# Kernel optimization log

Hardware: AMD Instinct MI355X
Metric: run time of the kernel (lower is better)

Reference implementation:

```python
import jax, jax.numpy as jnp
import numpy as np

# Assumptions from DCalhas/eeg_to_fmri repo layers:
#  - RandomFourierFeatures: z = cos(x @ W + b) followed by layer normalization
#    over the feature axis (normalization='layer'), W/b trainable.
#  - Sinusoids: elementwise sin(x).

B, D, T, L = 64, 512, 1024, 512

def _layer_norm(x, eps=1e-5):
    mu = jnp.mean(x, axis=-1, keepdims=True)
    var = jnp.var(x, axis=-1, keepdims=True)
    return (x - mu) * jax.lax.rsqrt(var + eps)

def setup_inputs() -> dict:
    key = jax.random.key(0)
    ks = jax.random.split(key, 12)
    s = 1.0 / np.sqrt(L)
    return {
        "x": jax.random.normal(ks[0], (B, D, T), jnp.float32),
        "rff_w": jax.random.normal(ks[1], (D, L), jnp.float32) * (1.0 / np.sqrt(D)),
        "rff_b": jax.random.uniform(ks[2], (L,), jnp.float32, 0.0, 2.0 * np.pi),
        "weight_input": jax.random.normal(ks[3], (L, L), jnp.float32) * s,
        "weight_forget": jax.random.normal(ks[4], (L, L), jnp.float32) * s,
        "weight_context": jax.random.normal(ks[5], (L, L), jnp.float32) * s,
        "recurrent_input": jax.random.normal(ks[6], (L, L), jnp.float32) * s,
        "recurrent_forget": jax.random.normal(ks[7], (L, L), jnp.float32) * s,
        "recurrent_context": jax.random.normal(ks[8], (L, L), jnp.float32) * s,
        "bias_input": jnp.zeros((L,), jnp.float32),
        "bias_forget": jnp.zeros((L,), jnp.float32),
        "bias_context": jnp.zeros((L,), jnp.float32),
        "init_latent": jax.random.normal(ks[9], (1, 1, L), jnp.float32) * s,
        "init_context": jax.random.normal(ks[10], (1, 1, L), jnp.float32) * s,
    }

def reference(x, rff_w, rff_b, weight_input, weight_forget, weight_context,
              recurrent_input, recurrent_forget, recurrent_context,
              bias_input, bias_forget, bias_context, init_latent, init_context):
    b = x.shape[0]
    xt = jnp.transpose(x, (0, 2, 1))                      # [B,T,D]
    z = _layer_norm(jnp.cos(xt @ rff_w + rff_b))          # [B,T,L]
    # hidden_states[t+1] = z_t in the original loop, so the "recurrent" input
    # at step t is z_{t-1} (init_latent at t=0). Gates are thus batchable.
    z_prev = jnp.concatenate(
        [jnp.broadcast_to(init_latent, (b, 1, z.shape[2])), z[:, :-1]], axis=1)
    i = jax.nn.sigmoid(z @ weight_input + z_prev @ recurrent_input + bias_input)
    f = jax.nn.sigmoid(z @ weight_forget + z_prev @ recurrent_forget + bias_forget)
    g = jnp.tanh(z @ weight_context + z_prev @ recurrent_context + bias_context)
    o = jnp.sin(z)                                        # Sinusoids gate

    c0 = jnp.broadcast_to(init_context[:, 0], (b, z.shape[2]))  # [B,L]
    def step(c_prev, gates):
        i_t, f_t, g_t, o_t = gates
        c_t = f_t * c_prev + i_t * g_t
        return c_t, o_t * c_t
    xs = tuple(jnp.transpose(a, (1, 0, 2)) for a in (i, f, g, o))  # time-major
    _, h = jax.lax.scan(step, c0, xs)                     # [T,B,L]
    return jnp.transpose(h, (1, 2, 0))                    # [B,L,T]
```

## Files before the change

kernel.cpp:

```cpp
#include <hip/hip_runtime.h>
#include <hip/hip_bf16.h>
#include <hip/hip_fp16.h>
#include <cstdint>
#include <cstddef>


typedef float f32x4 __attribute__((ext_vector_type(4)));
typedef short s16x8 __attribute__((ext_vector_type(8)));

__device__ __forceinline__ void gload_lds16(const void* g, void* l) {
  __builtin_amdgcn_global_load_lds(
      (const __attribute__((address_space(1))) void*)g,
      (__attribute__((address_space(3))) void*)l, 16, 0, 0);
}
__device__ __forceinline__ ushort f2bf(float f) {
  uint32_t u = __float_as_uint(f);
  return (ushort)((u + 0x7FFF + ((u >> 16) & 1)) >> 16);
}
__device__ __forceinline__ float bf2f(ushort s) {
  return __uint_as_float(((uint32_t)s) << 16);
}
__device__ __forceinline__ ushort f2h(float f) {
  return __half_as_ushort(__float2half(f));
}
__device__ __forceinline__ float h2f(ushort s) {
  return __half2float(__ushort_as_half(s));
}

#define MF(d, a, b) d = __builtin_amdgcn_mfma_f32_16x16x32_bf16(a, b, d, 0, 0, 0);

__global__ __launch_bounds__(256) void transpose_cvt(
    const float* __restrict__ src, ushort* __restrict__ dst, int ld)
{
  __shared__ float tile[32][33];
  const int c0 = blockIdx.x * 32, r0 = blockIdx.y * 32;
  const int tx = threadIdx.x & 31, ty = threadIdx.x >> 5;
#pragma unroll
  for (int i = 0; i < 4; ++i)
    tile[ty + i * 8][tx] = src[(size_t)(r0 + ty + i * 8) * 512 + c0 + tx];
  __syncthreads();
#pragma unroll
  for (int i = 0; i < 4; ++i)
    dst[(size_t)(c0 + ty + i * 8) * ld + r0 + tx] = f2bf(tile[tx][ty + i * 8]);
}

__global__ __launch_bounds__(256) void transpose6(
    const float* __restrict__ s0, const float* __restrict__ s1,
    const float* __restrict__ s2, const float* __restrict__ s3,
    const float* __restrict__ s4, const float* __restrict__ s5,
    const float* __restrict__ il, ushort* __restrict__ W2t,
    ushort* __restrict__ ilb)
{
  const int z = blockIdx.z;
  if (z == 6) {
    if (blockIdx.x == 0 && blockIdx.y == 0) {
      ilb[threadIdx.x] = f2bf(il[threadIdx.x]);
      ilb[threadIdx.x + 256] = f2bf(il[threadIdx.x + 256]);
    }
    return;
  }
  const float* src = z == 0 ? s0 : z == 1 ? s1 : z == 2 ? s2
                   : z == 3 ? s3 : z == 4 ? s4 : s5;
  ushort* dst = W2t + (size_t)(z >> 1) * 512 * 1024 + (z & 1) * 512;
  __shared__ float tile[32][33];
  const int c0 = blockIdx.x * 32, r0 = blockIdx.y * 32;
  const int tx = threadIdx.x & 31, ty = threadIdx.x >> 5;
#pragma unroll
  for (int i = 0; i < 4; ++i)
    tile[ty + i * 8][tx] = src[(size_t)(r0 + ty + i * 8) * 512 + c0 + tx];
  __syncthreads();
#pragma unroll
  for (int i = 0; i < 4; ++i)
    dst[(size_t)(c0 + ty + i * 8) * 1024 + r0 + tx] = f2bf(tile[tx][ty + i * 8]);
}

__global__ __launch_bounds__(256) void transpose_x(
    const float* __restrict__ x, ushort* __restrict__ xt)
{
  __shared__ float tile[64][68];
  const int b = blockIdx.z;
  const int t0 = blockIdx.x * 64, d0 = blockIdx.y * 64;
  const float* src = x + ((size_t)b * 512 + d0) * 1024 + t0;
  const int lr_ = threadIdx.x >> 4, lc4 = (threadIdx.x & 15) * 4;
#pragma unroll
  for (int p = 0; p < 4; ++p) {
    const float4 v = *(const float4*)(src + (size_t)(lr_ + p * 16) * 1024 + lc4);
    *(float4*)&tile[lr_ + p * 16][lc4] = v;
  }
  __syncthreads();
  const int tt = threadIdx.x >> 2, dc = (threadIdx.x & 3) * 16;
  ushort* dst = xt + ((size_t)b * 1024 + t0 + tt) * 512 + d0 + dc;
  uint4 o1, o2;
  o1.x = (uint)f2bf(tile[dc + 0][tt]) | ((uint)f2bf(tile[dc + 1][tt]) << 16);
  o1.y = (uint)f2bf(tile[dc + 2][tt]) | ((uint)f2bf(tile[dc + 3][tt]) << 16);
  o1.z = (uint)f2bf(tile[dc + 4][tt]) | ((uint)f2bf(tile[dc + 5][tt]) << 16);
  o1.w = (uint)f2bf(tile[dc + 6][tt]) | ((uint)f2bf(tile[dc + 7][tt]) << 16);
  o2.x = (uint)f2bf(tile[dc + 8][tt]) | ((uint)f2bf(tile[dc + 9][tt]) << 16);
  o2.y = (uint)f2bf(tile[dc + 10][tt]) | ((uint)f2bf(tile[dc + 11][tt]) << 16);
  o2.z = (uint)f2bf(tile[dc + 12][tt]) | ((uint)f2bf(tile[dc + 13][tt]) << 16);
  o2.w = (uint)f2bf(tile[dc + 14][tt]) | ((uint)f2bf(tile[dc + 15][tt]) << 16);
  *(uint4*)(dst) = o1;
  *(uint4*)(dst + 8) = o2;
}

__global__ __launch_bounds__(256, 2) void k1_mfma(
    const ushort* __restrict__ A, const ushort* __restrict__ Bt,
    const float* __restrict__ bias, ushort* __restrict__ U)
{
  __shared__ __align__(16) short As[128 * 64];
  __shared__ __align__(16) short Bs[128 * 64];
  const int tid = threadIdx.x;
  const int lane = tid & 63, wid = tid >> 6;
  const int orig = blockIdx.x;
  const int swz = (orig & 7) * 256 + (orig >> 3);
  const int n0 = (swz & 3) * 128, r0 = (swz >> 2) * 128;
  const int wr = wid >> 1, wc = wid & 1;
  const int fr = lane & 15, fq = lane >> 4;
  const int lr = lane >> 3;
  const int swz_el = ((lane & 7) ^ lr) * 8;

  const int RA = r0 + wid * 32 + lr;
  const ushort* pa0 = A + (size_t)(RA)      * 512 + swz_el;
  const ushort* pa1 = A + (size_t)(RA + 8)  * 512 + swz_el;
  const ushort* pa2 = A + (size_t)(RA + 16) * 512 + swz_el;
  const ushort* pa3 = A + (size_t)(RA + 24) * 512 + swz_el;
  const int RB = n0 + wid * 32 + lr;
  const ushort* pb0 = Bt + (size_t)(RB)      * 512 + swz_el;
  const ushort* pb1 = Bt + (size_t)(RB + 8)  * 512 + swz_el;
  const ushort* pb2 = Bt + (size_t)(RB + 16) * 512 + swz_el;
  const ushort* pb3 = Bt + (size_t)(RB + 24) * 512 + swz_el;
  char* dA = (char*)As + wid * 4096;
  char* dB = (char*)Bs + wid * 4096;

  const int so0 = fr * 64 + ((fq)     ^ (fr & 7)) * 8;
  const int so1 = fr * 64 + ((4 + fq) ^ (fr & 7)) * 8;

  f32x4 c00 = {0.f,0.f,0.f,0.f}, c01 = c00, c02 = c00, c03 = c00,
        c10 = c00, c11 = c00, c12 = c00, c13 = c00,
        c20 = c00, c21 = c00, c22 = c00, c23 = c00,
        c30 = c00, c31 = c00, c32 = c00, c33 = c00;

  for (int k0 = 0; k0 < 512; k0 += 64) {
    gload_lds16(pa0 + k0, dA);        gload_lds16(pa1 + k0, dA + 1024);
    gload_lds16(pa2 + k0, dA + 2048); gload_lds16(pa3 + k0, dA + 3072);
    gload_lds16(pb0 + k0, dB);        gload_lds16(pb1 + k0, dB + 1024);
    gload_lds16(pb2 + k0, dB + 2048); gload_lds16(pb3 + k0, dB + 3072);
    __syncthreads();
    const s16x8 a00 = *(const s16x8*)&As[wr * 4096 + 0 * 1024 + so0];
    const s16x8 a01 = *(const s16x8*)&As[wr * 4096 + 0 * 1024 + so1];
    const s16x8 a10 = *(const s16x8*)&As[wr * 4096 + 1 * 1024 + so0];
    const s16x8 a11 = *(const s16x8*)&As[wr * 4096 + 1 * 1024 + so1];
    const s16x8 a20 = *(const s16x8*)&As[wr * 4096 + 2 * 1024 + so0];
    const s16x8 a21 = *(const s16x8*)&As[wr * 4096 + 2 * 1024 + so1];
    const s16x8 a30 = *(const s16x8*)&As[wr * 4096 + 3 * 1024 + so0];
    const s16x8 a31 = *(const s16x8*)&As[wr * 4096 + 3 * 1024 + so1];
    const s16x8 b00 = *(const s16x8*)&Bs[wc * 4096 + 0 * 1024 + so0];
    const s16x8 b01 = *(const s16x8*)&Bs[wc * 4096 + 0 * 1024 + so1];
    const s16x8 b10 = *(const s16x8*)&Bs[wc * 4096 + 1 * 1024 + so0];
    const s16x8 b11 = *(const s16x8*)&Bs[wc * 4096 + 1 * 1024 + so1];
    const s16x8 b20 = *(const s16x8*)&Bs[wc * 4096 + 2 * 1024 + so0];
    const s16x8 b21 = *(const s16x8*)&Bs[wc * 4096 + 2 * 1024 + so1];
    const s16x8 b30 = *(const s16x8*)&Bs[wc * 4096 + 3 * 1024 + so0];
    const s16x8 b31 = *(const s16x8*)&Bs[wc * 4096 + 3 * 1024 + so1];
    MF(c00, a00, b00) MF(c01, a00, b10) MF(c02, a00, b20) MF(c03, a00, b30)
    MF(c10, a10, b00) MF(c11, a10, b10) MF(c12, a10, b20) MF(c13, a10, b30)
    MF(c20, a20, b00) MF(c21, a20, b10) MF(c22, a20, b20) MF(c23, a20, b30)
    MF(c30, a30, b00) MF(c31, a30, b10) MF(c32, a30, b20) MF(c33, a30, b30)
    MF(c00, a01, b01) MF(c01, a01, b11) MF(c02, a01, b21) MF(c03, a01, b31)
    MF(c10, a11, b01) MF(c11, a11, b11) MF(c12, a11, b21) MF(c13, a11, b31)
    MF(c20, a21, b01) MF(c21, a21, b11) MF(c22, a21, b21) MF(c23, a21, b31)
    MF(c30, a31, b01) MF(c31, a31, b11) MF(c32, a31, b21) MF(c33, a31, b31)
    __syncthreads();
  }

#define EPI1(cmn, m_, n_) { \
    const int col = n0 + wc * 64 + n_ * 16 + fr; \
    const float bv = bias[col]; \
    const int rbase = r0 + wr * 64 + m_ * 16 + fq * 4; \
    _Pragma("unroll") for (int j = 0; j < 4; ++j) \
      U[(size_t)(rbase + j) * 512 + col] = f2bf(cosf(cmn[j] + bv)); }
  EPI1(c00, 0, 0) EPI1(c01, 0, 1) EPI1(c02, 0, 2) EPI1(c03, 0, 3)
  EPI1(c10, 1, 0) EPI1(c11, 1, 1) EPI1(c12, 1, 2) EPI1(c13, 1, 3)
  EPI1(c20, 2, 0) EPI1(c21, 2, 1) EPI1(c22, 2, 2) EPI1(c23, 2, 3)
  EPI1(c30, 3, 0) EPI1(c31, 3, 1) EPI1(c32, 3, 2) EPI1(c33, 3, 3)
#undef EPI1
}

__global__ __launch_bounds__(256) void ln_rows(
    const ushort* __restrict__ U, ushort* __restrict__ Z)
{
  const int row = blockIdx.x * 4 + (threadIdx.x >> 6);
  const int lane = threadIdx.x & 63;
  const size_t base = (size_t)row * 512 + lane * 8;
  const uint4 pk = *(const uint4*)(U + base);
  float v[8];
  v[0] = bf2f(pk.x & 0xffff); v[1] = bf2f(pk.x >> 16);
  v[2] = bf2f(pk.y & 0xffff); v[3] = bf2f(pk.y >> 16);
  v[4] = bf2f(pk.z & 0xffff); v[5] = bf2f(pk.z >> 16);
  v[6] = bf2f(pk.w & 0xffff); v[7] = bf2f(pk.w >> 16);
  float s = 0.f, s2 = 0.f;
#pragma unroll
  for (int j = 0; j < 8; ++j) { s += v[j]; s2 += v[j] * v[j]; }
#pragma unroll
  for (int m = 1; m < 64; m <<= 1) { s += __shfl_xor(s, m); s2 += __shfl_xor(s2, m); }
  const float mean = s * (1.f / 512.f);
  const float var = s2 * (1.f / 512.f) - mean * mean;
  const float inv = rsqrtf(var + 1e-5f);
  uint4 o;
  o.x = (uint)f2bf((v[0] - mean) * inv) | ((uint)f2bf((v[1] - mean) * inv) << 16);
  o.y = (uint)f2bf((v[2] - mean) * inv) | ((uint)f2bf((v[3] - mean) * inv) << 16);
  o.z = (uint)f2bf((v[4] - mean) * inv) | ((uint)f2bf((v[5] - mean) * inv) << 16);
  o.w = (uint)f2bf((v[6] - mean) * inv) | ((uint)f2bf((v[7] - mean) * inv) << 16);
  *(uint4*)(Z + base) = o;
}

__global__ __launch_bounds__(256, 2) void k2_mfma(
    const ushort* __restrict__ Z, const ushort* __restrict__ Wt,
    const ushort* __restrict__ IL,
    const float* __restrict__ b0v, const float* __restrict__ b1v,
    const float* __restrict__ b2v,
    ushort* __restrict__ gates, int tc, int Tc, int nwg)
{
  __shared__ __align__(16) short As[128 * 64];
  __shared__ __align__(16) short Bs[128 * 64];
  const int tid = threadIdx.x;
  const int lane = tid & 63, wid = tid >> 6;
  const int cpx = nwg >> 3;
  const int orig = blockIdx.x;
  const int swz = (orig & 7) * cpx + (orig >> 3);
  const int bx = swz % 12, by = swz / 12;
  const int nb = Tc >> 7;
  const int b = by / nb, tb = by % nb;
  const int r0g = b * 1024 + tc + tb * 128;
  const int r0c = b * Tc + tb * 128;
  const int n0 = bx * 128;
  const int wr = wid >> 1, wc = wid & 1;
  const int fr = lane & 15, fq = lane >> 4;
  const int lr = lane >> 3;
  const int swz_el = ((lane & 7) ^ lr) * 8;

  const int R0 = r0g + wid * 32 + lr;
  const ushort* pa0 = Z + (size_t)(R0)      * 512 + swz_el;
  const ushort* pa1 = Z + (size_t)(R0 + 8)  * 512 + swz_el;
  const ushort* pa2 = Z + (size_t)(R0 + 16) * 512 + swz_el;
  const ushort* pa3 = Z + (size_t)(R0 + 24) * 512 + swz_el;
  const ushort* ph0 = ((((R0)      & 1023) == 0) ? IL : (Z + (size_t)(R0 - 1)  * 512)) + swz_el;
  const ushort* ph1 = ((((R0 + 8)  & 1023) == 0) ? IL : (Z + (size_t)(R0 + 7)  * 512)) + swz_el;
  const ushort* ph2 = ((((R0 + 16) & 1023) == 0) ? IL : (Z + (size_t)(R0 + 15) * 512)) + swz_el;
  const ushort* ph3 = ((((R0 + 24) & 1023) == 0) ? IL : (Z + (size_t)(R0 + 23) * 512)) + swz_el;
  const int RB = n0 + wid * 32 + lr;
  const ushort* pb0 = Wt + (size_t)(RB)      * 1024 + swz_el;
  const ushort* pb1 = Wt + (size_t)(RB + 8)  * 1024 + swz_el;
  const ushort* pb2 = Wt + (size_t)(RB + 16) * 1024 + swz_el;
  const ushort* pb3 = Wt + (size_t)(RB + 24) * 1024 + swz_el;
  char* dA = (char*)As + wid * 4096;
  char* dB = (char*)Bs + wid * 4096;

  const int so0 = fr * 64 + ((fq)     ^ (fr & 7)) * 8;
  const int so1 = fr * 64 + ((4 + fq) ^ (fr & 7)) * 8;

  f32x4 c00 = {0.f,0.f,0.f,0.f}, c01 = c00, c02 = c00, c03 = c00,
        c10 = c00, c11 = c00, c12 = c00, c13 = c00,
        c20 = c00, c21 = c00, c22 = c00, c23 = c00,
        c30 = c00, c31 = c00, c32 = c00, c33 = c00;

#define K2BODY \
    __syncthreads(); \
    { \
    const s16x8 a00 = *(const s16x8*)&As[wr * 4096 + 0 * 1024 + so0]; \
    const s16x8 a01 = *(const s16x8*)&As[wr * 4096 + 0 * 1024 + so1]; \
    const s16x8 a10 = *(const s16x8*)&As[wr * 4096 + 1 * 1024 + so0]; \
    const s16x8 a11 = *(const s16x8*)&As[wr * 4096 + 1 * 1024 + so1]; \
    const s16x8 a20 = *(const s16x8*)&As[wr * 4096 + 2 * 1024 + so0]; \
    const s16x8 a21 = *(const s16x8*)&As[wr * 4096 + 2 * 1024 + so1]; \
    const s16x8 a30 = *(const s16x8*)&As[wr * 4096 + 3 * 1024 + so0]; \
    const s16x8 a31 = *(const s16x8*)&As[wr * 4096 + 3 * 1024 + so1]; \
    const s16x8 b00 = *(const s16x8*)&Bs[wc * 4096 + 0 * 1024 + so0]; \
    const s16x8 b01 = *(const s16x8*)&Bs[wc * 4096 + 0 * 1024 + so1]; \
    const s16x8 b10 = *(const s16x8*)&Bs[wc * 4096 + 1 * 1024 + so0]; \
    const s16x8 b11 = *(const s16x8*)&Bs[wc * 4096 + 1 * 1024 + so1]; \
    const s16x8 b20 = *(const s16x8*)&Bs[wc * 4096 + 2 * 1024 + so0]; \
    const s16x8 b21 = *(const s16x8*)&Bs[wc * 4096 + 2 * 1024 + so1]; \
    const s16x8 b30 = *(const s16x8*)&Bs[wc * 4096 + 3 * 1024 + so0]; \
    const s16x8 b31 = *(const s16x8*)&Bs[wc * 4096 + 3 * 1024 + so1]; \
    MF(c00, a00, b00) MF(c01, a00, b10) MF(c02, a00, b20) MF(c03, a00, b30) \
    MF(c10, a10, b00) MF(c11, a10, b10) MF(c12, a10, b20) MF(c13, a10, b30) \
    MF(c20, a20, b00) MF(c21, a20, b10) MF(c22, a20, b20) MF(c23, a20, b30) \
    MF(c30, a30, b00) MF(c31, a30, b10) MF(c32, a30, b20) MF(c33, a30, b30) \
    MF(c00, a01, b01) MF(c01, a01, b11) MF(c02, a01, b21) MF(c03, a01, b31) \
    MF(c10, a11, b01) MF(c11, a11, b11) MF(c12, a11, b21) MF(c13, a11, b31) \
    MF(c20, a21, b01) MF(c21, a21, b11) MF(c22, a21, b21) MF(c23, a21, b31) \
    MF(c30, a31, b01) MF(c31, a31, b11) MF(c32, a31, b21) MF(c33, a31, b31) \
    } \
    __syncthreads();

  for (int k0 = 0; k0 < 512; k0 += 64) {
    gload_lds16(pa0 + k0, dA);        gload_lds16(pa1 + k0, dA + 1024);
    gload_lds16(pa2 + k0, dA + 2048); gload_lds16(pa3 + k0, dA + 3072);
    gload_lds16(pb0 + k0, dB);        gload_lds16(pb1 + k0, dB + 1024);
    gload_lds16(pb2 + k0, dB + 2048); gload_lds16(pb3 + k0, dB + 3072);
    K2BODY
  }
  for (int k0 = 0; k0 < 512; k0 += 64) {
    gload_lds16(ph0 + k0, dA);        gload_lds16(ph1 + k0, dA + 1024);
    gload_lds16(ph2 + k0, dA + 2048); gload_lds16(ph3 + k0, dA + 3072);
    gload_lds16(pb0 + 512 + k0, dB);        gload_lds16(pb1 + 512 + k0, dB + 1024);
    gload_lds16(pb2 + 512 + k0, dB + 2048); gload_lds16(pb3 + 512 + k0, dB + 3072);
    K2BODY
  }
#undef K2BODY

  const int sel = n0 >> 9;
  const float* bb = sel == 0 ? b0v : (sel == 1 ? b1v : b2v);
#define EPI(cmn, m_, n_) { \
    const int col = n0 + wc * 64 + n_ * 16 + fr; \
    const float bv = bb[col & 511]; \
    const int rbase = wr * 64 + m_ * 16 + fq * 4; \
    _Pragma("unroll") for (int j = 0; j < 4; ++j) { \
      const float uu = cmn[j] + bv; \
      const float vv = (sel < 2) ? (1.f / (1.f + __expf(-uu))) \
                                 : (2.f / (1.f + __expf(-2.f * uu)) - 1.f); \
      gates[(size_t)(r0c + rbase + j) * 1536 + col] = f2h(vv); } }
  EPI(c00, 0, 0) EPI(c01, 0, 1) EPI(c02, 0, 2) EPI(c03, 0, 3)
  EPI(c10, 1, 0) EPI(c11, 1, 1) EPI(c12, 1, 2) EPI(c13, 1, 3)
  EPI(c20, 2, 0) EPI(c21, 2, 1) EPI(c22, 2, 2) EPI(c23, 2, 3)
  EPI(c30, 3, 0) EPI(c31, 3, 1) EPI(c32, 3, 2) EPI(c33, 3, 3)
#undef EPI
}

__global__ __launch_bounds__(256) void k3a_seg(
    const ushort* __restrict__ gates, float* __restrict__ Aseg,
    float* __restrict__ Bseg, int Tc)
{
  const int l = blockIdx.x * 256 + threadIdx.x;
  const int b = blockIdx.y, s = blockIdx.z;
  const int SEGc = Tc >> 6;
  const ushort* gb = gates + ((size_t)(b * Tc + s * 64)) * 1536 + l;
  float A = 1.f, c = 0.f;
#pragma unroll 8
  for (int j = 0; j < 64; ++j) {
    const float iv = h2f(gb[(size_t)j * 1536]);
    const float fv = h2f(gb[(size_t)j * 1536 + 512]);
    const float gv = h2f(gb[(size_t)j * 1536 + 1024]);
    A *= fv;
    c = fmaf(fv, c, iv * gv);
  }
  const size_t o = (size_t)(b * SEGc + s) * 512 + l;
  Aseg[o] = A;
  Bseg[o] = c;
}

__global__ __launch_bounds__(512) void k3b_comb(
    const float* __restrict__ Aseg, const float* __restrict__ Bseg,
    const float* __restrict__ initc, float* __restrict__ cstart,
    float* __restrict__ cbuf, int tc, int Tc)
{
  const int b = blockIdx.x, l = threadIdx.x;
  const int SEGc = Tc >> 6;
  float c = (tc == 0) ? initc[l] : cbuf[b * 512 + l];
  for (int s = 0; s < SEGc; ++s) {
    const size_t o = (size_t)(b * SEGc + s) * 512 + l;
    cstart[o] = c;
    c = fmaf(Aseg[o], c, Bseg[o]);
  }
  cbuf[b * 512 + l] = c;
}

__global__ __launch_bounds__(128) void k3c_emit(
    const ushort* __restrict__ gates, const ushort* __restrict__ Z,
    const float* __restrict__ cstart, float* __restrict__ out,
    int tc, int Tc)
{
  __shared__ float tile[128][65];
  const int tid = threadIdx.x;
  const int l0 = blockIdx.x * 128;
  const int b = blockIdx.y, s = blockIdx.z;
  const int SEGc = Tc >> 6;
  const int l = l0 + tid;

  float c = cstart[(size_t)(b * SEGc + s) * 512 + l];
  const ushort* gb = gates + ((size_t)(b * Tc + s * 64)) * 1536 + l;
  const ushort* zb = Z + ((size_t)(b * 1024 + tc + s * 64)) * 512 + l;
#pragma unroll 8
  for (int j = 0; j < 64; ++j) {
    const float iv = h2f(gb[(size_t)j * 1536]);
    const float fv = h2f(gb[(size_t)j * 1536 + 512]);
    const float gv = h2f(gb[(size_t)j * 1536 + 1024]);
    const float zv = bf2f(zb[(size_t)j * 512]);
    c = fmaf(fv, c, iv * gv);
    tile[tid][j] = sinf(zv) * c;
  }
  __syncthreads();
  const int col = tid & 63, rhalf = tid >> 6;
  const size_t obase = ((size_t)b * 512 + l0) * 1024 + (size_t)(tc + s * 64) + col;
#pragma unroll
  for (int p = 0; p < 64; ++p) {
    const int row = rhalf + p * 2;
    out[obase + (size_t)row * 1024] = tile[row][col];
  }
}

extern "C" void kernel_launch(void* const* d_in, const int* in_sizes, int n_in,
                              void* d_out, int out_size, void* d_ws, size_t ws_size,
                              hipStream_t stream)
{
  const float* x  = (const float*)d_in[0];
  const float* W  = (const float*)d_in[1];
  const float* rb = (const float*)d_in[2];
  const float* wi = (const float*)d_in[3];
  const float* wf = (const float*)d_in[4];
  const float* wc = (const float*)d_in[5];
  const float* ri = (const float*)d_in[6];
  const float* rf = (const float*)d_in[7];
  const float* rc = (const float*)d_in[8];
  const float* bi = (const float*)d_in[9];
  const float* bfo = (const float*)d_in[10];
  const float* bc = (const float*)d_in[11];
  const float* il = (const float*)d_in[12];
  const float* ic = (const float*)d_in[13];
  float* out = (float*)d_out;

  char* ws = (char*)d_ws;
  size_t off = 0;
  auto alloc = [&](size_t bytes) -> void* {
    void* p = ws + off;
    off = (off + bytes + 255) & ~(size_t)255;
    return p;
  };
  ushort* z    = (ushort*)alloc((size_t)65536 * 512 * 2);
  ushort* W1t  = (ushort*)alloc((size_t)512 * 512 * 2);
  ushort* W2t  = (ushort*)alloc((size_t)1536 * 1024 * 2);
  ushort* ilb  = (ushort*)alloc(512 * 2);
  float*  cbuf = (float*)alloc((size_t)64 * 512 * 4);
  float*  Aseg = (float*)alloc((size_t)64 * 16 * 512 * 4);
  float*  Bseg = (float*)alloc((size_t)64 * 16 * 512 * 4);
  float*  cstart = (float*)alloc((size_t)64 * 16 * 512 * 4);
  const size_t fixed_end = off;
  ushort* xt   = (ushort*)alloc((size_t)65536 * 512 * 2);
  ushort* gates = (ushort*)(ws + fixed_end);
  ushort* u    = (ushort*)d_out;

  int Tc = 1024;
  while (Tc > 128 && fixed_end + (size_t)64 * Tc * 1536 * 2 > ws_size) Tc >>= 1;

  transpose_cvt<<<dim3(16, 16), 256, 0, stream>>>(W, W1t, 512);
  transpose6<<<dim3(16, 16, 7), 256, 0, stream>>>(wi, ri, wf, rf, wc, rc, il, W2t, ilb);
  transpose_x<<<dim3(16, 8, 64), 256, 0, stream>>>(x, xt);

  k1_mfma<<<dim3(2048), 256, 0, stream>>>(xt, W1t, rb, u);
  ln_rows<<<16384, 256, 0, stream>>>(u, z);

  for (int tc = 0; tc < 1024; tc += Tc) {
    const int SEGc = Tc >> 6;
    const int nwg2 = 12 * 64 * (Tc >> 7);
    k2_mfma<<<dim3(nwg2), 256, 0, stream>>>(
        z, W2t, ilb, bi, bfo, bc, gates, tc, Tc, nwg2);
    k3a_seg<<<dim3(2, 64, SEGc), 256, 0, stream>>>(gates, Aseg, Bseg, Tc);
    k3b_comb<<<64, 512, 0, stream>>>(Aseg, Bseg, ic, cstart, cbuf, tc, Tc);
    k3c_emit<<<dim3(4, 64, SEGc), 128, 0, stream>>>(gates, z, cstart, out, tc, Tc);
  }
}
```

Before: 606.9 us.

## Double-buffer LDS tiles in gate GEMM to overlap global loads with MFMA

After: 655.9 us. +8.1%, slower.

```diff
diff --git a/kernel.cpp b/kernel.cpp
--- a/kernel.cpp
+++ b/kernel.cpp
@@ -221,8 +221,8 @@
     const float* __restrict__ b2v,
     ushort* __restrict__ gates, int tc, int Tc, int nwg)
 {
-  __shared__ __align__(16) short As[128 * 64];
-  __shared__ __align__(16) short Bs[128 * 64];
+  __shared__ __align__(16) short As[2][128 * 64];
+  __shared__ __align__(16) short Bs[2][128 * 64];
   const int tid = threadIdx.x;
   const int lane = tid & 63, wid = tid >> 6;
   const int cpx = nwg >> 3;
@@ -253,62 +253,68 @@
   const ushort* pb1 = Wt + (size_t)(RB + 8)  * 1024 + swz_el;
   const ushort* pb2 = Wt + (size_t)(RB + 16) * 1024 + swz_el;
   const ushort* pb3 = Wt + (size_t)(RB + 24) * 1024 + swz_el;
-  char* dA = (char*)As + wid * 4096;
-  char* dB = (char*)Bs + wid * 4096;
-
-  const int so0 = fr * 64 + ((fq)     ^ (fr & 7)) * 8;
-  const int so1 = fr * 64 + ((4 + fq) ^ (fr & 7)) * 8;
-
-  f32x4 c00 = {0.f,0.f,0.f,0.f}, c01 = c00, c02 = c00, c03 = c00,
-        c10 = c00, c11 = c00, c12 = c00, c13 = c00,
-        c20 = c00, c21 = c00, c22 = c00, c23 = c00,
-        c30 = c00, c31 = c00, c32 = c00, c33 = c00;
-
-#define K2BODY \
-    __syncthreads(); \
-    { \
-    const s16x8 a00 = *(const s16x8*)&As[wr * 4096 + 0 * 1024 + so0]; \
-    const s16x8 a01 = *(const s16x8*)&As[wr * 4096 + 0 * 1024 + so1]; \
-    const s16x8 a10 = *(const s16x8*)&As[wr * 4096 + 1 * 1024 + so0]; \
-    const s16x8 a11 = *(const s16x8*)&As[wr * 4096 + 1 * 1024 + so1]; \
-    const s16x8 a20 = *(const s16x8*)&As[wr * 4096 + 2 * 1024 + so0]; \
-    const s16x8 a21 = *(const s16x8*)&As[wr * 4096 + 2 * 1024 + so1]; \
-    const s16x8 a30 = *(const s16x8*)&As[wr * 4096 + 3 * 1024 + so0]; \
-    const s16x8 a31 = *(const s16x8*)&As[wr * 4096 + 3 * 1024 + so1]; \
-    const s16x8 b00 = *(const s16x8*)&Bs[wc * 4096 + 0 * 1024 + so0]; \
-    const s16x8 b01 = *(const s16x8*)&Bs[wc * 4096 + 0 * 1024 + so1]; \
-    const s16x8 b10 = *(const s16x8*)&Bs[wc * 4096 + 1 * 1024 + so0]; \
-    const s16x8 b11 = *(const s16x8*)&Bs[wc * 4096 + 1 * 1024 + so1]; \
-    const s16x8 b20 = *(const s16x8*)&Bs[wc * 4096 + 2 * 1024 + so0]; \
-    const s16x8 b21 = *(const s16x8*)&Bs[wc * 4096 + 2 * 1024 + so1]; \
-    const s16x8 b30 = *(const s16x8*)&Bs[wc * 4096 + 3 * 1024 + so0]; \
-    const s16x8 b31 = *(const s16x8*)&Bs[wc * 4096 + 3 * 1024 + so1]; \
-    MF(c00, a00, b00) MF(c01, a00, b10) MF(c02, a00, b20) MF(c03, a00, b30) \
-    MF(c10, a10, b00) MF(c11, a10, b10) MF(c12, a10, b20) MF(c13, a10, b30) \
-    MF(c20, a20, b00) MF(c21, a20, b10) MF(c22, a20, b20) MF(c23, a20, b30) \
-    MF(c30, a30, b00) MF(c31, a30, b10) MF(c32, a30, b20) MF(c33, a30, b30) \
-    MF(c00, a01, b01) MF(c01, a01, b11) MF(c02, a01, b21) MF(c03, a01, b31) \
-    MF(c10, a11, b01) MF(c11, a11, b11) MF(c12, a11, b21) MF(c13, a11, b31) \
-    MF(c20, a21, b01) MF(c21, a21, b11) MF(c22, a21, b21) MF(c23, a21, b31) \
-    MF(c30, a31, b01) MF(c31, a31, b11) MF(c32, a31, b21) MF(c33, a31, b31) \
-    } \
-    __syncthreads();
-
-  for (int k0 = 0; k0 < 512; k0 += 64) {
-    gload_lds16(pa0 + k0, dA);        gload_lds16(pa1 + k0, dA + 1024);
-    gload_lds16(pa2 + k0, dA + 2048); gload_lds16(pa3 + k0, dA + 3072);
-    gload_lds16(pb0 + k0, dB);        gload_lds16(pb1 + k0, dB + 1024);
-    gload_lds16(pb2 + k0, dB + 2048); gload_lds16(pb3 + k0, dB + 3072);
-    K2BODY
-  }
-  for (int k0 = 0; k0 < 512; k0 += 64) {
-    gload_lds16(ph0 + k0, dA);        gload_lds16(ph1 + k0, dA + 1024);
-    gload_lds16(ph2 + k0, dA + 2048); gload_lds16(ph3 + k0, dA + 3072);
-    gload_lds16(pb0 + 512 + k0, dB);        gload_lds16(pb1 + 512 + k0, dB + 1024);
-    gload_lds16(pb2 + 512 + k0, dB + 2048); gload_lds16(pb3 + 512 + k0, dB + 3072);
-    K2BODY
-  }
-#undef K2BODY
+
+#define STG(kt_, BUF_) { \
+    char* dA = (char*)As + (BUF_) * 16384 + wid * 4096; \
+    char* dB = (char*)Bs + (BUF_) * 16384 + wid * 4096; \
+    if ((kt_) < 8) { const int ko = (kt_) * 64; \
+      gload_lds16(pa0 + ko, dA);        gload_lds16(pa1 + ko, dA + 1024); \
+      gload_lds16(pa2 + ko, dA + 2048); gload_lds16(pa3 + ko, dA + 3072); \
+    } else { const int ko = ((kt_) - 8) * 64; \
+      gload_lds16(ph0 + ko, dA);        gload_lds16(ph1 + ko, dA + 1024); \
+      gload_lds16(ph2 + ko, dA + 2048); gload_lds16(ph3 + ko, dA + 3072); } \
+    { const int kb = (kt_) * 64; \
+      gload_lds16(pb0 + kb, dB);        gload_lds16(pb1 + kb, dB + 1024); \
+      gload_lds16(pb2 + kb, dB + 2048); gload_lds16(pb3 + kb, dB + 3072); } }
+
+  f32x4 zz = {0.f,0.f,0.f,0.f};
+  f32x4 c00=zz,c01=zz,c02=zz,c03=zz, c10=zz,c11=zz,c12=zz,c13=zz,
+        c20=zz,c21=zz,c22=zz,c23=zz, c30=zz,c31=zz,c32=zz,c33=zz;
+  s16x8 fa0, fa1, fa2, fa3, fb0, fb1, fb2, fb3;
+
+#define RD(BUF_, KS_) { \
+    const int so = fr * 64 + (((KS_) * 4 + fq) ^ (fr & 7)) * 8; \
+    const short* A_ = &As[BUF_][0]; \
+    const short* B_ = &Bs[BUF_][0]; \
+    fa0 = *(const s16x8*)&A_[wr * 4096 + 0 * 1024 + so]; \
+    fa1 = *(const s16x8*)&A_[wr * 4096 + 1 * 1024 + so]; \
+    fa2 = *(const s16x8*)&A_[wr * 4096 + 2 * 1024 + so]; \
+    fa3 = *(const s16x8*)&A_[wr * 4096 + 3 * 1024 + so]; \
+    fb0 = *(const s16x8*)&B_[wc * 4096 + 0 * 1024 + so]; \
+    fb1 = *(const s16x8*)&B_[wc * 4096 + 1 * 1024 + so]; \
+    fb2 = *(const s16x8*)&B_[wc * 4096 + 2 * 1024 + so]; \
+    fb3 = *(const s16x8*)&B_[wc * 4096 + 3 * 1024 + so]; }
+
+#define MM \
+    MF(c00,fa0,fb0) MF(c01,fa0,fb1) MF(c02,fa0,fb2) MF(c03,fa0,fb3) \
+    MF(c10,fa1,fb0) MF(c11,fa1,fb1) MF(c12,fa1,fb2) MF(c13,fa1,fb3) \
+    MF(c20,fa2,fb0) MF(c21,fa2,fb1) MF(c22,fa2,fb2) MF(c23,fa2,fb3) \
+    MF(c30,fa3,fb0) MF(c31,fa3,fb1) MF(c32,fa3,fb2) MF(c33,fa3,fb3)
+
+  STG(0, 0)
+  asm volatile("s_waitcnt vmcnt(0)" ::: "memory");
+  __builtin_amdgcn_s_barrier();
+  __builtin_amdgcn_sched_barrier(0);
+#pragma unroll
+  for (int kt = 0; kt < 16; ++kt) {
+    const int cur = kt & 1;
+    if (kt < 15) { STG(kt + 1, cur ^ 1) }
+    RD(cur, 0)
+    __builtin_amdgcn_s_setprio(1);
+    MM
+    __builtin_amdgcn_s_setprio(0);
+    RD(cur, 1)
+    __builtin_amdgcn_s_setprio(1);
+    MM
+    __builtin_amdgcn_s_setprio(0);
+    __builtin_amdgcn_sched_barrier(0);
+    asm volatile("s_waitcnt vmcnt(0)" ::: "memory");
+    __builtin_amdgcn_s_barrier();
+    __builtin_amdgcn_sched_barrier(0);
+  }
+#undef MM
+#undef RD
+#undef STG
 
   const int sel = n0 >> 9;
   const float* bb = sel == 0 ? b0v : (sel == 1 ? b1v : b2v);
```

## Fuse input and context gates into one product in the gate GEMM epilogue

Applied to the files above, without the earlier changes.

New measurement: 568.1 us. 1.07x faster.

```diff
diff --git a/kernel.cpp b/kernel.cpp
--- a/kernel.cpp
+++ b/kernel.cpp
@@ -217,23 +217,25 @@
 __global__ __launch_bounds__(256, 2) void k2_mfma(
     const ushort* __restrict__ Z, const ushort* __restrict__ Wt,
     const ushort* __restrict__ IL,
-    const float* __restrict__ b0v, const float* __restrict__ b1v,
-    const float* __restrict__ b2v,
-    ushort* __restrict__ gates, int tc, int Tc, int nwg)
+    const float* __restrict__ biv, const float* __restrict__ bfv,
+    const float* __restrict__ bcv,
+    ushort* __restrict__ G2, int tc, int Tc, int nwg)
 {
   __shared__ __align__(16) short As[128 * 64];
-  __shared__ __align__(16) short Bs[128 * 64];
+  __shared__ __align__(16) short Bs0[128 * 64];
+  __shared__ __align__(16) short Bs1[128 * 64];
   const int tid = threadIdx.x;
   const int lane = tid & 63, wid = tid >> 6;
   const int cpx = nwg >> 3;
   const int orig = blockIdx.x;
   const int swz = (orig & 7) * cpx + (orig >> 3);
-  const int bx = swz % 12, by = swz / 12;
+  const int bx = swz & 7, by = swz >> 3;
   const int nb = Tc >> 7;
   const int b = by / nb, tb = by % nb;
   const int r0g = b * 1024 + tc + tb * 128;
   const int r0c = b * Tc + tb * 128;
-  const int n0 = bx * 128;
+  const bool isig = bx < 4;
+  const int n0 = (bx & 3) * 128;
   const int wr = wid >> 1, wc = wid & 1;
   const int fr = lane & 15, fq = lane >> 4;
   const int lr = lane >> 3;
@@ -248,102 +250,130 @@
   const ushort* ph1 = ((((R0 + 8)  & 1023) == 0) ? IL : (Z + (size_t)(R0 + 7)  * 512)) + swz_el;
   const ushort* ph2 = ((((R0 + 16) & 1023) == 0) ? IL : (Z + (size_t)(R0 + 15) * 512)) + swz_el;
   const ushort* ph3 = ((((R0 + 24) & 1023) == 0) ? IL : (Z + (size_t)(R0 + 23) * 512)) + swz_el;
-  const int RB = n0 + wid * 32 + lr;
-  const ushort* pb0 = Wt + (size_t)(RB)      * 1024 + swz_el;
-  const ushort* pb1 = Wt + (size_t)(RB + 8)  * 1024 + swz_el;
-  const ushort* pb2 = Wt + (size_t)(RB + 16) * 1024 + swz_el;
-  const ushort* pb3 = Wt + (size_t)(RB + 24) * 1024 + swz_el;
-  char* dA = (char*)As + wid * 4096;
-  char* dB = (char*)Bs + wid * 4096;
+  const int RB0 = (isig ? n0 : 512 + n0) + wid * 32 + lr;
+  const ushort* pb0 = Wt + (size_t)(RB0)      * 1024 + swz_el;
+  const ushort* pb1 = Wt + (size_t)(RB0 + 8)  * 1024 + swz_el;
+  const ushort* pb2 = Wt + (size_t)(RB0 + 16) * 1024 + swz_el;
+  const ushort* pb3 = Wt + (size_t)(RB0 + 24) * 1024 + swz_el;
+  const int RB1 = 1024 + n0 + wid * 32 + lr;
+  const ushort* pq0 = Wt + (size_t)(RB1)      * 1024 + swz_el;
+  const ushort* pq1 = Wt + (size_t)(RB1 + 8)  * 1024 + swz_el;
+  const ushort* pq2 = Wt + (size_t)(RB1 + 16) * 1024 + swz_el;
+  const ushort* pq3 = Wt + (size_t)(RB1 + 24) * 1024 + swz_el;
 
   const int so0 = fr * 64 + ((fq)     ^ (fr & 7)) * 8;
   const int so1 = fr * 64 + ((4 + fq) ^ (fr & 7)) * 8;
 
-  f32x4 c00 = {0.f,0.f,0.f,0.f}, c01 = c00, c02 = c00, c03 = c00,
-        c10 = c00, c11 = c00, c12 = c00, c13 = c00,
-        c20 = c00, c21 = c00, c22 = c00, c23 = c00,
-        c30 = c00, c31 = c00, c32 = c00, c33 = c00;
-
-#define K2BODY \
-    __syncthreads(); \
-    { \
-    const s16x8 a00 = *(const s16x8*)&As[wr * 4096 + 0 * 1024 + so0]; \
-    const s16x8 a01 = *(const s16x8*)&As[wr * 4096 + 0 * 1024 + so1]; \
-    const s16x8 a10 = *(const s16x8*)&As[wr * 4096 + 1 * 1024 + so0]; \
-    const s16x8 a11 = *(const s16x8*)&As[wr * 4096 + 1 * 1024 + so1]; \
-    const s16x8 a20 = *(const s16x8*)&As[wr * 4096 + 2 * 1024 + so0]; \
-    const s16x8 a21 = *(const s16x8*)&As[wr * 4096 + 2 * 1024 + so1]; \
-    const s16x8 a30 = *(const s16x8*)&As[wr * 4096 + 3 * 1024 + so0]; \
-    const s16x8 a31 = *(const s16x8*)&As[wr * 4096 + 3 * 1024 + so1]; \
-    const s16x8 b00 = *(const s16x8*)&Bs[wc * 4096 + 0 * 1024 + so0]; \
-    const s16x8 b01 = *(const s16x8*)&Bs[wc * 4096 + 0 * 1024 + so1]; \
-    const s16x8 b10 = *(const s16x8*)&Bs[wc * 4096 + 1 * 1024 + so0]; \
-    const s16x8 b11 = *(const s16x8*)&Bs[wc * 4096 + 1 * 1024 + so1]; \
-    const s16x8 b20 = *(const s16x8*)&Bs[wc * 4096 + 2 * 1024 + so0]; \
-    const s16x8 b21 = *(const s16x8*)&Bs[wc * 4096 + 2 * 1024 + so1]; \
-    const s16x8 b30 = *(const s16x8*)&Bs[wc * 4096 + 3 * 1024 + so0]; \
-    const s16x8 b31 = *(const s16x8*)&Bs[wc * 4096 + 3 * 1024 + so1]; \
-    MF(c00, a00, b00) MF(c01, a00, b10) MF(c02, a00, b20) MF(c03, a00, b30) \
-    MF(c10, a10, b00) MF(c11, a10, b10) MF(c12, a10, b20) MF(c13, a10, b30) \
-    MF(c20, a20, b00) MF(c21, a20, b10) MF(c22, a20, b20) MF(c23, a20, b30) \
-    MF(c30, a30, b00) MF(c31, a30, b10) MF(c32, a30, b20) MF(c33, a30, b30) \
-    MF(c00, a01, b01) MF(c01, a01, b11) MF(c02, a01, b21) MF(c03, a01, b31) \
-    MF(c10, a11, b01) MF(c11, a11, b11) MF(c12, a11, b21) MF(c13, a11, b31) \
-    MF(c20, a21, b01) MF(c21, a21, b11) MF(c22, a21, b21) MF(c23, a21, b31) \
-    MF(c30, a31, b01) MF(c31, a31, b11) MF(c32, a31, b21) MF(c33, a31, b31) \
-    } \
-    __syncthreads();
+  f32x4 zz = {0.f,0.f,0.f,0.f};
+  f32x4 c00=zz,c01=zz,c02=zz,c03=zz, c10=zz,c11=zz,c12=zz,c13=zz,
+        c20=zz,c21=zz,c22=zz,c23=zz, c30=zz,c31=zz,c32=zz,c33=zz;
+  f32x4 d00=zz,d01=zz,d02=zz,d03=zz, d10=zz,d11=zz,d12=zz,d13=zz,
+        d20=zz,d21=zz,d22=zz,d23=zz, d30=zz,d31=zz,d32=zz,d33=zz;
+
+#define STG8(P0,P1,P2,P3, KO, DST) { \
+    char* d_ = (char*)(DST) + wid * 4096; \
+    gload_lds16((P0) + (KO), d_);        gload_lds16((P1) + (KO), d_ + 1024); \
+    gload_lds16((P2) + (KO), d_ + 2048); gload_lds16((P3) + (KO), d_ + 3072); }
+
+#define RDA(SO) \
+    const s16x8 fa0 = *(const s16x8*)&As[wr * 4096 + 0 * 1024 + (SO)]; \
+    const s16x8 fa1 = *(const s16x8*)&As[wr * 4096 + 1 * 1024 + (SO)]; \
+    const s16x8 fa2 = *(const s16x8*)&As[wr * 4096 + 2 * 1024 + (SO)]; \
+    const s16x8 fa3 = *(const s16x8*)&As[wr * 4096 + 3 * 1024 + (SO)];
+
+#define RDB(BS, SO) \
+    const s16x8 fb0 = *(const s16x8*)&(BS)[wc * 4096 + 0 * 1024 + (SO)]; \
+    const s16x8 fb1 = *(const s16x8*)&(BS)[wc * 4096 + 1 * 1024 + (SO)]; \
+    const s16x8 fb2 = *(const s16x8*)&(BS)[wc * 4096 + 2 * 1024 + (SO)]; \
+    const s16x8 fb3 = *(const s16x8*)&(BS)[wc * 4096 + 3 * 1024 + (SO)];
+
+#define MMC \
+    MF(c00,fa0,fb0) MF(c01,fa0,fb1) MF(c02,fa0,fb2) MF(c03,fa0,fb3) \
+    MF(c10,fa1,fb0) MF(c11,fa1,fb1) MF(c12,fa1,fb2) MF(c13,fa1,fb3) \
+    MF(c20,fa2,fb0) MF(c21,fa2,fb1) MF(c22,fa2,fb2) MF(c23,fa2,fb3) \
+    MF(c30,fa3,fb0) MF(c31,fa3,fb1) MF(c32,fa3,fb2) MF(c33,fa3,fb3)
+
+#define MMD \
+    MF(d00,fa0,fb0) MF(d01,fa0,fb1) MF(d02,fa0,fb2) MF(d03,fa0,fb3) \
+    MF(d10,fa1,fb0) MF(d11,fa1,fb1) MF(d12,fa1,fb2) MF(d13,fa1,fb3) \
+    MF(d20,fa2,fb0) MF(d21,fa2,fb1) MF(d22,fa2,fb2) MF(d23,fa2,fb3) \
+    MF(d30,fa3,fb0) MF(d31,fa3,fb1) MF(d32,fa3,fb2) MF(d33,fa3,fb3)
+
+#define KSTEP(SO_) { \
+    RDA(SO_) \
+    { RDB(Bs0, SO_) MMC } \
+    if (isig) { RDB(Bs1, SO_) MMD } }
 
   for (int k0 = 0; k0 < 512; k0 += 64) {
-    gload_lds16(pa0 + k0, dA);        gload_lds16(pa1 + k0, dA + 1024);
-    gload_lds16(pa2 + k0, dA + 2048); gload_lds16(pa3 + k0, dA + 3072);
-    gload_lds16(pb0 + k0, dB);        gload_lds16(pb1 + k0, dB + 1024);
-    gload_lds16(pb2 + k0, dB + 2048); gload_lds16(pb3 + k0, dB + 3072);
-    K2BODY
+    STG8(pa0, pa1, pa2, pa3, k0, As)
+    STG8(pb0, pb1, pb2, pb3, k0, Bs0)
+    if (isig) { STG8(pq0, pq1, pq2, pq3, k0, Bs1) }
+    __syncthreads();
+    KSTEP(so0)
+    KSTEP(so1)
+    __syncthreads();
   }
   for (int k0 = 0; k0 < 512; k0 += 64) {
-    gload_lds16(ph0 + k0, dA);        gload_lds16(ph1 + k0, dA + 1024);
-    gload_lds16(ph2 + k0, dA + 2048); gload_lds16(ph3 + k0, dA + 3072);
-    gload_lds16(pb0 + 512 + k0, dB);        gload_lds16(pb1 + 512 + k0, dB + 1024);
-    gload_lds16(pb2 + 512 + k0, dB + 2048); gload_lds16(pb3 + 512 + k0, dB + 3072);
-    K2BODY
-  }
-#undef K2BODY
-
-  const int sel = n0 >> 9;
-  const float* bb = sel == 0 ? b0v : (sel == 1 ? b1v : b2v);
+    STG8(ph0, ph1, ph2, ph3, k0, As)
+    STG8(pb0, pb1, pb2, pb3, 512 + k0, Bs0)
+    if (isig) { STG8(pq0, pq1, pq2, pq3, 512 + k0, Bs1) }
+    __syncthreads();
+    KSTEP(so0)
+    KSTEP(so1)
+    __syncthreads();
+  }
+#undef KSTEP
+#undef MMD
+#undef MMC
+#undef RDB
+#undef RDA
+#undef STG8
+
+  if (isig) {
+#define EPI(cmn, dmn, m_, n_) { \
+    const int col = n0 + wc * 64 + n_ * 16 + fr; \
+    const float bvi = biv[col], bvc = bcv[col]; \
+    const int rbase = wr * 64 + m_ * 16 + fq * 4; \
+    _Pragma("unroll") for (int j = 0; j < 4; ++j) { \
+      const float iv = 1.f / (1.f + __expf(-(cmn[j] + bvi))); \
+      const float gv = 2.f / (1.f + __expf(-2.f * (dmn[j] + bvc))) - 1.f; \
+      G2[(size_t)(r0c + rbase + j) * 1024 + col] = f2h(iv * gv); } }
+    EPI(c00, d00, 0, 0) EPI(c01, d01, 0, 1) EPI(c02, d02, 0, 2) EPI(c03, d03, 0, 3)
+    EPI(c10, d10, 1, 0) EPI(c11, d11, 1, 1) EPI(c12, d12, 1, 2) EPI(c13, d13, 1, 3)
+    EPI(c20, d20, 2, 0) EPI(c21, d21, 2, 1) EPI(c22, d22, 2, 2) EPI(c23, d23, 2, 3)
+    EPI(c30, d30, 3, 0) EPI(c31, d31, 3, 1) EPI(c32, d32, 3, 2) EPI(c33, d33, 3, 3)
+#undef EPI
+  } else {
 #define EPI(cmn, m_, n_) { \
     const int col = n0 + wc * 64 + n_ * 16 + fr; \
-    const float bv = bb[col & 511]; \
+    const float bv = bfv[col]; \
     const int rbase = wr * 64 + m_ * 16 + fq * 4; \
     _Pragma("unroll") for (int j = 0; j < 4; ++j) { \
-      const float uu = cmn[j] + bv; \
-      const float vv = (sel < 2) ? (1.f / (1.f + __expf(-uu))) \
-                                 : (2.f / (1.f + __expf(-2.f * uu)) - 1.f); \
-      gates[(size_t)(r0c + rbase + j) * 1536 + col] = f2h(vv); } }
-  EPI(c00, 0, 0) EPI(c01, 0, 1) EPI(c02, 0, 2) EPI(c03, 0, 3)
-  EPI(c10, 1, 0) EPI(c11, 1, 1) EPI(c12, 1, 2) EPI(c13, 1, 3)
-  EPI(c20, 2, 0) EPI(c21, 2, 1) EPI(c22, 2, 2) EPI(c23, 2, 3)
-  EPI(c30, 3, 0) EPI(c31, 3, 1) EPI(c32, 3, 2) EPI(c33, 3, 3)
+      const float fv = 1.f / (1.f + __expf(-(cmn[j] + bv))); \
+      G2[(size_t)(r0c + rbase + j) * 1024 + 512 + col] = f2h(fv); } }
+    EPI(c00, 0, 0) EPI(c01, 0, 1) EPI(c02, 0, 2) EPI(c03, 0, 3)
+    EPI(c10, 1, 0) EPI(c11, 1, 1) EPI(c12, 1, 2) EPI(c13, 1, 3)
+    EPI(c20, 2, 0) EPI(c21, 2, 1) EPI(c22, 2, 2) EPI(c23, 2, 3)
+    EPI(c30, 3, 0) EPI(c31, 3, 1) EPI(c32, 3, 2) EPI(c33, 3, 3)
 #undef EPI
+  }
 }
 
 __global__ __launch_bounds__(256) void k3a_seg(
-    const ushort* __restrict__ gates, float* __restrict__ Aseg,
+    const ushort* __restrict__ G2, float* __restrict__ Aseg,
     float* __restrict__ Bseg, int Tc)
 {
   const int l = blockIdx.x * 256 + threadIdx.x;
   const int b = blockIdx.y, s = blockIdx.z;
   const int SEGc = Tc >> 6;
-  const ushort* gb = gates + ((size_t)(b * Tc + s * 64)) * 1536 + l;
+  const ushort* gb = G2 + ((size_t)(b * Tc + s * 64)) * 1024 + l;
   float A = 1.f, c = 0.f;
 #pragma unroll 8
   for (int j = 0; j < 64; ++j) {
-    const float iv = h2f(gb[(size_t)j * 1536]);
-    const float fv = h2f(gb[(size_t)j * 1536 + 512]);
-    const float gv = h2f(gb[(size_t)j * 1536 + 1024]);
-    A *= fv;
-    c = fmaf(fv, c, iv * gv);
+    const float P = h2f(gb[(size_t)j * 1024]);
+    const float F = h2f(gb[(size_t)j * 1024 + 512]);
+    A *= F;
+    c = fmaf(F, c, P);
   }
   const size_t o = (size_t)(b * SEGc + s) * 512 + l;
   Aseg[o] = A;
@@ -367,7 +397,7 @@
 }
 
 __global__ __launch_bounds__(128) void k3c_emit(
-    const ushort* __restrict__ gates, const ushort* __restrict__ Z,
+    const ushort* __restrict__ G2, const ushort* __restrict__ Z,
     const float* __restrict__ cstart, float* __restrict__ out,
     int tc, int Tc)
 {
@@ -379,15 +409,14 @@
   const int l = l0 + tid;
 
   float c = cstart[(size_t)(b * SEGc + s) * 512 + l];
-  const ushort* gb = gates + ((size_t)(b * Tc + s * 64)) * 1536 + l;
+  const ushort* gb = G2 + ((size_t)(b * Tc + s * 64)) * 1024 + l;
   const ushort* zb = Z + ((size_t)(b * 1024 + tc + s * 64)) * 512 + l;
 #pragma unroll 8
   for (int j = 0; j < 64; ++j) {
-    const float iv = h2f(gb[(size_t)j * 1536]);
-    const float fv = h2f(gb[(size_t)j * 1536 + 512]);
-    const float gv = h2f(gb[(size_t)j * 1536 + 1024]);
+    const float P = h2f(gb[(size_t)j * 1024]);
+    const float F = h2f(gb[(size_t)j * 1024 + 512]);
     const float zv = bf2f(zb[(size_t)j * 512]);
-    c = fmaf(fv, c, iv * gv);
+    c = fmaf(F, c, P);
     tile[tid][j] = sinf(zv) * c;
   }
   __syncthreads();
@@ -437,11 +466,11 @@
   float*  cstart = (float*)alloc((size_t)64 * 16 * 512 * 4);
   const size_t fixed_end = off;
   ushort* xt   = (ushort*)alloc((size_t)65536 * 512 * 2);
-  ushort* gates = (ushort*)(ws + fixed_end);
+  ushort* G2   = (ushort*)(ws + fixed_end);
   ushort* u    = (ushort*)d_out;
 
   int Tc = 1024;
-  while (Tc > 128 && fixed_end + (size_t)64 * Tc * 1536 * 2 > ws_size) Tc >>= 1;
+  while (Tc > 128 && fixed_end + (size_t)64 * Tc * 1024 * 2 > ws_size) Tc >>= 1;
 
   transpose_cvt<<<dim3(16, 16), 256, 0, stream>>>(W, W1t, 512);
   transpose6<<<dim3(16, 16, 7), 256, 0, stream>>>(wi, ri, wf, rf, wc, rc, il, W2t, ilb);
@@ -452,11 +481,11 @@
 
   for (int tc = 0; tc < 1024; tc += Tc) {
     const int SEGc = Tc >> 6;
-    const int nwg2 = 12 * 64 * (Tc >> 7);
+    const int nwg2 = 8 * 64 * (Tc >> 7);
     k2_mfma<<<dim3(nwg2), 256, 0, stream>>>(
-        z, W2t, ilb, bi, bfo, bc, gates, tc, Tc, nwg2);
-    k3a_seg<<<dim3(2, 64, SEGc), 256, 0, stream>>>(gates, Aseg, Bseg, Tc);
+        z, W2t, ilb, bi, bfo, bc, G2, tc, Tc, nwg2);
+    k3a_seg<<<dim3(2, 64, SEGc), 256, 0, stream>>>(G2, Aseg, Bseg, Tc);
     k3b_comb<<<64, 512, 0, stream>>>(Aseg, Bseg, ic, cstart, cbuf, tc, Tc);
-    k3c_emit<<<dim3(4, 64, SEGc), 128, 0, stream>>>(gates, z, cstart, out, tc, Tc);
-  }
-}
+    k3c_emit<<<dim3(4, 64, SEGc), 128, 0, stream>>>(G2, z, cstart, out, tc, Tc);
+  }
+}
```
